# Kernel tuning notes

Hardware: AMD Instinct MI355X
Metric: run time of the kernel (lower is better)

## Reference

```python
import jax, jax.numpy as jnp
import numpy as np

B, C, H, W = 32, 1024, 32, 32  # NOTE: code requires C == H*W (see bmm below)
C_HALF = C // 2


def setup_inputs() -> dict:
    key = jax.random.key(0)
    ks = jax.random.split(key, 7)
    s_in = 1.0 / np.sqrt(C)
    return {
        "x": jax.random.normal(ks[0], (B, C, H, W), dtype=jnp.float32),
        "Wq": jax.random.normal(ks[1], (C_HALF, C), dtype=jnp.float32) * s_in,
        "bq": jax.random.normal(ks[2], (C_HALF,), dtype=jnp.float32) * 0.01,
        "Wk": jax.random.normal(ks[3], (C_HALF, C), dtype=jnp.float32) * s_in,
        "bk": jax.random.normal(ks[4], (C_HALF,), dtype=jnp.float32) * 0.01,
        "Wv": jax.random.normal(ks[5], (C, C), dtype=jnp.float32) * s_in,
        "bv": jax.random.normal(ks[6], (C,), dtype=jnp.float32) * 0.01,
    }


def reference(x, Wq, bq, Wk, bk, Wv, bv):
    b, c, h, w = x.shape
    hw = h * w
    xf = x.reshape(b, c, hw)  # [B, C, HW]
    # 1x1 convs are per-pixel linear maps over channels
    q = jnp.einsum('oc,bcn->bno', Wq, xf) + bq            # [B, HW, C/2]  (permuted)
    k = jnp.einsum('oc,bcn->bon', Wk, xf) + bk[:, None]   # [B, C/2, HW]
    v = jnp.einsum('oc,bcn->bno', Wv, xf) + bv            # [B, HW, C]   (permuted)
    attn = jax.nn.softmax(jnp.einsum('bno,bom->bnm', q, k), axis=-1)  # [B, HW, HW]
    # torch: bmm(value [B,HW,C], attention^T [B,HW,HW]) -> requires C == HW
    out = jnp.einsum('bik,bjk->bij', v, attn)  # [B, HW(=C), HW]
    out = out.reshape(b, c, h, w)
    return out + x
```

## Files before the change

kernel.cpp:

```cpp
#include <hip/hip_runtime.h>

typedef _Float16 f16;
typedef _Float16 f16x8 __attribute__((ext_vector_type(8)));
typedef float f32x16 __attribute__((ext_vector_type(16)));

__device__ __forceinline__ void g2lds16(const void* g, void* l) {
    __builtin_amdgcn_global_load_lds(
        (const __attribute__((address_space(1))) void*)g,
        (__attribute__((address_space(3))) void*)l, 16, 0, 0);
}

__global__ __launch_bounds__(256)
void prep_w(const float* __restrict__ Wq, const float* __restrict__ bq,
            const float* __restrict__ Wk, const float* __restrict__ bk,
            const float* __restrict__ Wv, const float* __restrict__ bv,
            f16* __restrict__ Wall, float* __restrict__ ball)
{
    const int idx = blockIdx.x * 256 + threadIdx.x;
    const int o = idx >> 10;
    const int c = idx & 1023;
    float w;
    if (o < 512)        w = Wq[idx];
    else if (o < 1024)  w = Wk[idx - 512 * 1024];
    else                w = Wv[idx - 1024 * 1024];
    Wall[idx] = (f16)w;
    if (c == 0)
        ball[o] = (o < 512) ? bq[o] : (o < 1024) ? bk[o - 512] : bv[o - 1024];
}

__global__ __launch_bounds__(256)
void transpose_cast(const float* __restrict__ x, f16* __restrict__ xT)
{
    __shared__ float t[64][65];
    const int b  = blockIdx.z;
    const int c0 = blockIdx.y << 6;
    const int n0 = blockIdx.x << 6;
    const int tid = threadIdx.x;
    const float* xb = x + (unsigned long long)b * (1024ull * 1024ull);

    {
        const int cl = tid >> 4;
        const int n4 = (tid & 15) << 2;
#pragma unroll
        for (int i = 0; i < 64; i += 16) {
            const float4 v = *(const float4*)(xb + (unsigned long long)(c0 + cl + i) * 1024ull + (n0 + n4));
            t[cl + i][n4 + 0] = v.x; t[cl + i][n4 + 1] = v.y;
            t[cl + i][n4 + 2] = v.z; t[cl + i][n4 + 3] = v.w;
        }
    }
    __syncthreads();
    {
        f16* ob = xT + (unsigned long long)b * (1024ull * 1024ull);
        const int nl = tid >> 3;
        const int c8 = (tid & 7) << 3;
#pragma unroll
        for (int i = 0; i < 64; i += 32) {
            f16x8 h;
#pragma unroll
            for (int j = 0; j < 8; ++j) h[j] = (f16)t[c8 + j][nl + i];
            *(f16x8*)(ob + (unsigned long long)(n0 + nl + i) * 1024ull + (c0 + c8)) = h;
        }
    }
}

template <int EPI, int LDA, int LDB, int K, int LDO,
          long long SA, long long SB, long long SO, int SWZ>
__global__ __launch_bounds__(256, 4)
void gemm_nt(const f16* __restrict__ A, const f16* __restrict__ Bm,
             const float* __restrict__ bias,
             f16* __restrict__ Oh, float* __restrict__ Of,
             const float* __restrict__ Xres)
{
    __shared__ f16 As[128 * 64];
    __shared__ f16 Bs[128 * 64];

    const int tid  = threadIdx.x;
    const int wave = tid >> 6;
    const int lane = tid & 63;
    const int l31  = lane & 31;
    const int half = lane >> 5;
    const int wr   = (wave >> 1) << 6;
    const int wc   = (wave & 1) << 6;

    int bm, bn;
    if (SWZ) {
        const int xcd   = blockIdx.x & 7;
        const int local = blockIdx.x >> 3;
        const int stl   = local >> 5;
        const int sub   = local & 31;
        const int bng   = xcd & 1;
        const int g4    = stl * 4 + (xcd >> 1);
        bm = (g4 * 4 + (sub & 3)) << 7;
        bn = (bng * 8 + (sub >> 2)) << 7;
    } else {
        bm = blockIdx.x << 7;
        bn = blockIdx.y << 7;
    }
    const int bz = blockIdx.z;

    const f16* Ab = A  + (unsigned long long)bz * (unsigned long long)SA;
    const f16* Bb = Bm + (unsigned long long)bz * (unsigned long long)SB;

    const int srow = lane >> 3;
    const int scol = (((lane & 7) ^ srow) << 3);

    f32x16 acc[2][2] = {};

    for (int k0 = 0; k0 < K; k0 += 64) {
        __syncthreads();
#pragma unroll
        for (int t = 0; t < 4; ++t) {
            const int rb = t * 32 + wave * 8;
            g2lds16(Ab + (unsigned long long)(bm + rb + srow) * LDA + (k0 + scol),
                    As + rb * 64 + lane * 8);
            g2lds16(Bb + (unsigned long long)(bn + rb + srow) * LDB + (k0 + scol),
                    Bs + rb * 64 + lane * 8);
        }
        __syncthreads();

#pragma unroll
        for (int ks = 0; ks < 4; ++ks) {
            const int kg = ks * 2 + half;
            f16x8 af[2], bf[2];
#pragma unroll
            for (int i = 0; i < 2; ++i) {
                const int ra = wr + i * 32 + l31;
                af[i] = *(const f16x8*)(As + ra * 64 + ((kg ^ (ra & 7)) << 3));
                const int rbn = wc + i * 32 + l31;
                bf[i] = *(const f16x8*)(Bs + rbn * 64 + ((kg ^ (rbn & 7)) << 3));
            }
#pragma unroll
            for (int mi = 0; mi < 2; ++mi)
#pragma unroll
                for (int ni = 0; ni < 2; ++ni)
                    acc[mi][ni] = __builtin_amdgcn_mfma_f32_32x32x16_f16(
                        af[mi], bf[ni], acc[mi][ni], 0, 0, 0);
        }
    }

#pragma unroll
    for (int mi = 0; mi < 2; ++mi) {
#pragma unroll
        for (int ni = 0; ni < 2; ++ni) {
            const int col = bn + wc + ni * 32 + l31;
            float bc = 0.0f;
            if (EPI == 0) bc = bias[col];
#pragma unroll
            for (int r = 0; r < 16; ++r) {
                const int row = bm + wr + mi * 32 + (r & 3) + 8 * (r >> 2) + 4 * half;
                const float val = acc[mi][ni][r];
                if (EPI == 0) {
                    Oh[(unsigned long long)row * LDO + col] = (f16)(val + bc);
                } else if (EPI == 1) {
                    Of[(unsigned long long)bz * (unsigned long long)SO +
                       (unsigned long long)row * LDO + col] = val;
                } else {
                    const unsigned long long off =
                        (unsigned long long)bz * (unsigned long long)SO +
                        (unsigned long long)row * LDO + col;
                    Of[off] = val + Xres[off];
                }
            }
        }
    }
}

__global__ __launch_bounds__(256)
void softmax_rows(const float* __restrict__ S, f16* __restrict__ P)
{
    const unsigned long long row = blockIdx.x;
    const int tid = threadIdx.x;
    const float4 v = ((const float4*)(S + row * 1024ull))[tid];

    float m = fmaxf(fmaxf(v.x, v.y), fmaxf(v.z, v.w));
#pragma unroll
    for (int off = 32; off; off >>= 1)
        m = fmaxf(m, __shfl_xor(m, off, 64));

    __shared__ float redm[4], reds[4];
    const int wave = tid >> 6, lane = tid & 63;
    if (lane == 0) redm[wave] = m;
    __syncthreads();
    m = fmaxf(fmaxf(redm[0], redm[1]), fmaxf(redm[2], redm[3]));

    const float e0 = __expf(v.x - m), e1 = __expf(v.y - m);
    const float e2 = __expf(v.z - m), e3 = __expf(v.w - m);
    float sum = e0 + e1 + e2 + e3;
#pragma unroll
    for (int off = 32; off; off >>= 1)
        sum += __shfl_xor(sum, off, 64);
    if (lane == 0) reds[wave] = sum;
    __syncthreads();
    sum = reds[0] + reds[1] + reds[2] + reds[3];
    const float inv = 1.0f / sum;

    union { f16 h[4]; uint2 u; } pk;
    pk.h[0] = (f16)(e0 * inv); pk.h[1] = (f16)(e1 * inv);
    pk.h[2] = (f16)(e2 * inv); pk.h[3] = (f16)(e3 * inv);
    ((uint2*)(P + row * 1024ull))[tid] = pk.u;
}

extern "C" void kernel_launch(void* const* d_in, const int* in_sizes, int n_in,
                              void* d_out, int out_size, void* d_ws, size_t ws_size,
                              hipStream_t stream)
{
    const float* x  = (const float*)d_in[0];
    const float* Wq = (const float*)d_in[1];
    const float* bq = (const float*)d_in[2];
    const float* Wk = (const float*)d_in[3];
    const float* bk = (const float*)d_in[4];
    const float* Wv = (const float*)d_in[5];
    const float* bv = (const float*)d_in[6];
    float* out = (float*)d_out;

    f16*   xT   = (f16*)d_ws;
    f16*   Wall = xT + 32ull * 1024 * 1024;
    float* ball = (float*)(Wall + 2048ull * 1024);
    f16*   QKV  = (f16*)(ball + 2048);
    float* S    = (float*)(QKV + 64ull * 1024 * 1024);
    f16*   P    = (f16*)(S + 32ull * 1024 * 1024);

    prep_w<<<8192, 256, 0, stream>>>(Wq, bq, Wk, bk, Wv, bv, Wall, ball);
    transpose_cast<<<dim3(16, 16, 32), 256, 0, stream>>>(x, xT);

    gemm_nt<0, 1024, 1024, 1024, 2048, 0ll, 0ll, 0ll, 1>
        <<<dim3(4096, 1, 1), 256, 0, stream>>>(
        xT, Wall, ball, QKV, nullptr, nullptr);

    gemm_nt<1, 2048, 2048, 512, 1024, 1024ll * 2048, 1024ll * 2048, 1024ll * 1024, 0>
        <<<dim3(8, 8, 32), 256, 0, stream>>>(
        QKV, QKV + 512, nullptr, nullptr, S, nullptr);

    softmax_rows<<<32768, 256, 0, stream>>>(S, P);

    gemm_nt<2, 2048, 1024, 1024, 1024, 1024ll * 2048, 1024ll * 1024, 1024ll * 1024, 0>
        <<<dim3(8, 8, 32), 256, 0, stream>>>(
        QKV + 1024, P, nullptr, nullptr, out, x);
}
```

Baseline: 612.0 us.

## Fuse QK^T GEMM with row softmax and swizzle final GEMM blocks per XCD

Replaces the separate QK^T GEMM (fp32 score matrix written to global) and the row-softmax kernel with one kernel. Each 512-thread block computes a 32-row by 1024-key score tile in registers with Q held in LDS and K streamed through it, then runs a cross-wave max/sum reduction and writes fp16 probabilities directly. This removes the 128 MB fp32 S round trip and one launch. It also adds an XCD-aware block swizzle to the final PV GEMM so the tiles of each batch stay on one XCD for L2 reuse. The trade-off is that the fused kernel uses 1024 blocks with large LDS per block (about 96 KB), which lowers occupancy and may leave MFMA units underused.

```diff
diff --git a/kernel.cpp b/kernel.cpp
--- a/kernel.cpp
+++ b/kernel.cpp
@@ -82,8 +82,8 @@
     const int wr   = (wave >> 1) << 6;
     const int wc   = (wave & 1) << 6;
 
-    int bm, bn;
-    if (SWZ) {
+    int bm, bn, bz = blockIdx.z;
+    if (SWZ == 1) {
         const int xcd   = blockIdx.x & 7;
         const int local = blockIdx.x >> 3;
         const int stl   = local >> 5;
@@ -92,11 +92,20 @@
         const int g4    = stl * 4 + (xcd >> 1);
         bm = (g4 * 4 + (sub & 3)) << 7;
         bn = (bng * 8 + (sub >> 2)) << 7;
+    } else if (SWZ == 2) {
+        const int xcd   = blockIdx.x & 7;
+        const int local = blockIdx.x >> 3;
+        const int unit  = local >> 5;
+        const int wi    = local & 31;
+        const int pp    = unit * 8 + xcd;
+        bz = pp >> 1;
+        const int bh = pp & 1;
+        bm = (wi & 7) << 7;
+        bn = ((bh << 2) + (wi >> 3)) << 7;
     } else {
         bm = blockIdx.x << 7;
         bn = blockIdx.y << 7;
     }
-    const int bz = blockIdx.z;
 
     const f16* Ab = A  + (unsigned long long)bz * (unsigned long long)SA;
     const f16* Bb = Bm + (unsigned long long)bz * (unsigned long long)SB;
@@ -165,39 +174,135 @@
     }
 }
 
-__global__ __launch_bounds__(256)
-void softmax_rows(const float* __restrict__ S, f16* __restrict__ P)
-{
-    const unsigned long long row = blockIdx.x;
-    const int tid = threadIdx.x;
-    const float4 v = ((const float4*)(S + row * 1024ull))[tid];
-
-    float m = fmaxf(fmaxf(v.x, v.y), fmaxf(v.z, v.w));
-#pragma unroll
-    for (int off = 32; off; off >>= 1)
-        m = fmaxf(m, __shfl_xor(m, off, 64));
-
-    __shared__ float redm[4], reds[4];
-    const int wave = tid >> 6, lane = tid & 63;
-    if (lane == 0) redm[wave] = m;
+__global__ __launch_bounds__(512)
+void qk_softmax(const f16* __restrict__ QKV, f16* __restrict__ P)
+{
+    __shared__ f16 Qs[32 * 512];
+    __shared__ f16 Ks[512 * 64];
+    __shared__ float redm[8][2][16];
+    __shared__ float reds[8][2][16];
+
+    const int tid  = threadIdx.x;
+    const int wave = tid >> 6;
+    const int lane = tid & 63;
+    const int l31  = lane & 31;
+    const int half = lane >> 5;
+
+    const int xcd   = blockIdx.x & 7;
+    const int local = blockIdx.x >> 3;
+    const int batch = xcd * 4 + (local >> 5);
+    const int jt    = local & 31;
+    const int j0    = jt << 5;
+
+    const f16* Qb = QKV + (unsigned long long)batch * (1024ull * 2048ull);
+    const f16* Kb = Qb + 512;
+
+#pragma unroll
+    for (int i = 0; i < 4; ++i) {
+        const int row = wave * 4 + i;
+        g2lds16(Qb + (unsigned long long)(j0 + row) * 2048ull + ((lane ^ (row & 7)) << 3),
+                Qs + row * 512 + lane * 8);
+    }
+
+    f32x16 acc[4] = {};
+    const int wkey = wave << 7;
+
+    for (int d0 = 0; d0 < 512; d0 += 32) {
+        __syncthreads();
+#pragma unroll
+        for (int t = 0; t < 8; ++t) {
+            const int rb  = wave * 64 + t * 8;
+            const int R   = rb + (lane >> 3);
+            const int p   = (lane & 7) ^ (R & 7);
+            const int key = (R << 1) + (p >> 2);
+            const int slt = p & 3;
+            g2lds16(Kb + (unsigned long long)key * 2048ull + d0 + (slt << 3),
+                    Ks + rb * 64 + lane * 8);
+        }
+        __syncthreads();
+#pragma unroll
+        for (int ks = 0; ks < 2; ++ks) {
+            const int sl = ks * 2 + half;
+            const int gs = (d0 >> 3) + sl;
+            const f16x8 af = *(const f16x8*)(Qs + l31 * 512 + ((gs ^ (l31 & 7)) << 3));
+#pragma unroll
+            for (int ni = 0; ni < 4; ++ni) {
+                const int key = wkey + ni * 32 + l31;
+                const int R   = key >> 1;
+                const int p   = ((key & 1) << 2) + sl;
+                const f16x8 bf = *(const f16x8*)(Ks + R * 64 + ((p ^ (R & 7)) << 3));
+                acc[ni] = __builtin_amdgcn_mfma_f32_32x32x16_f16(af, bf, acc[ni], 0, 0, 0);
+            }
+        }
+    }
+
+    float mx[16];
+#pragma unroll
+    for (int r = 0; r < 16; ++r) {
+        float m = fmaxf(fmaxf(acc[0][r], acc[1][r]), fmaxf(acc[2][r], acc[3][r]));
+#pragma unroll
+        for (int off = 16; off; off >>= 1)
+            m = fmaxf(m, __shfl_xor(m, off, 64));
+        mx[r] = m;
+    }
+    if (l31 == 0) {
+#pragma unroll
+        for (int r = 0; r < 16; ++r) redm[wave][half][r] = mx[r];
+    }
     __syncthreads();
-    m = fmaxf(fmaxf(redm[0], redm[1]), fmaxf(redm[2], redm[3]));
-
-    const float e0 = __expf(v.x - m), e1 = __expf(v.y - m);
-    const float e2 = __expf(v.z - m), e3 = __expf(v.w - m);
-    float sum = e0 + e1 + e2 + e3;
-#pragma unroll
-    for (int off = 32; off; off >>= 1)
-        sum += __shfl_xor(sum, off, 64);
-    if (lane == 0) reds[wave] = sum;
+#pragma unroll
+    for (int r = 0; r < 16; ++r) {
+        float m = redm[0][half][r];
+#pragma unroll
+        for (int w = 1; w < 8; ++w) m = fmaxf(m, redm[w][half][r]);
+        mx[r] = m;
+    }
+
+    float sm[16];
+#pragma unroll
+    for (int r = 0; r < 16; ++r) sm[r] = 0.0f;
+#pragma unroll
+    for (int ni = 0; ni < 4; ++ni)
+#pragma unroll
+        for (int r = 0; r < 16; ++r) {
+            const float e = __expf(acc[ni][r] - mx[r]);
+            acc[ni][r] = e;
+            sm[r] += e;
+        }
+#pragma unroll
+    for (int r = 0; r < 16; ++r) {
+#pragma unroll
+        for (int off = 16; off; off >>= 1)
+            sm[r] += __shfl_xor(sm[r], off, 64);
+    }
+    if (l31 == 0) {
+#pragma unroll
+        for (int r = 0; r < 16; ++r) reds[wave][half][r] = sm[r];
+    }
     __syncthreads();
-    sum = reds[0] + reds[1] + reds[2] + reds[3];
-    const float inv = 1.0f / sum;
-
-    union { f16 h[4]; uint2 u; } pk;
-    pk.h[0] = (f16)(e0 * inv); pk.h[1] = (f16)(e1 * inv);
-    pk.h[2] = (f16)(e2 * inv); pk.h[3] = (f16)(e3 * inv);
-    ((uint2*)(P + row * 1024ull))[tid] = pk.u;
+#pragma unroll
+    for (int r = 0; r < 16; ++r) {
+        float s = reds[0][half][r];
+#pragma unroll
+        for (int w = 1; w < 8; ++w) s += reds[w][half][r];
+        sm[r] = 1.0f / s;
+    }
+
+    f16* Pt = Ks;
+#pragma unroll
+    for (int ni = 0; ni < 4; ++ni)
+#pragma unroll
+        for (int r = 0; r < 16; ++r) {
+            const int row = (r & 3) + 8 * (r >> 2) + 4 * half;
+            const int key = wkey + ni * 32 + l31;
+            Pt[row * 1024 + key] = (f16)(acc[ni][r] * sm[r]);
+        }
+    __syncthreads();
+
+    f16* Pg = P + ((unsigned long long)batch * 1024ull + j0) * 1024ull;
+#pragma unroll
+    for (int i = 0; i < 8; ++i)
+        *(f16x8*)(Pg + i * 4096 + tid * 8) = *(const f16x8*)(Pt + i * 4096 + tid * 8);
 }
 
 extern "C" void kernel_launch(void* const* d_in, const int* in_sizes, int n_in,
@@ -217,8 +322,7 @@
     f16*   Wall = xT + 32ull * 1024 * 1024;
     float* ball = (float*)(Wall + 2048ull * 1024);
     f16*   QKV  = (f16*)(ball + 2048);
-    float* S    = (float*)(QKV + 64ull * 1024 * 1024);
-    f16*   P    = (f16*)(S + 32ull * 1024 * 1024);
+    f16*   P    = QKV + 64ull * 1024 * 1024;
 
     prep_w<<<8192, 256, 0, stream>>>(Wq, bq, Wk, bk, Wv, bv, Wall, ball);
     transpose_cast<<<dim3(16, 16, 32), 256, 0, stream>>>(x, xT);
@@ -227,13 +331,9 @@
         <<<dim3(4096, 1, 1), 256, 0, stream>>>(
         xT, Wall, ball, QKV, nullptr, nullptr);
 
-    gemm_nt<1, 2048, 2048, 512, 1024, 1024ll * 2048, 1024ll * 2048, 1024ll * 1024, 0>
-        <<<dim3(8, 8, 32), 256, 0, stream>>>(
-        QKV, QKV + 512, nullptr, nullptr, S, nullptr);
-
-    softmax_rows<<<32768, 256, 0, stream>>>(S, P);
-
-    gemm_nt<2, 2048, 1024, 1024, 1024, 1024ll * 2048, 1024ll * 1024, 1024ll * 1024, 0>
-        <<<dim3(8, 8, 32), 256, 0, stream>>>(
+    qk_softmax<<<dim3(1024, 1, 1), 512, 0, stream>>>(QKV, P);
+
+    gemm_nt<2, 2048, 1024, 1024, 1024, 1024ll * 2048, 1024ll * 1024, 1024ll * 1024, 2>
+        <<<dim3(2048, 1, 1), 256, 0, stream>>>(
         QKV + 1024, P, nullptr, nullptr, out, x);
 }
```

Result: slower. 650.4 us (+6.3%).
